# Kernel optimization log

Measured on AMD Instinct MI355X. Metric: run time of the kernel, lower is better.

## Reference

```python
import jax, jax.numpy as jnp
import numpy as np
from jax.ops import segment_sum

EPS = 1e-5
N, E = 100000, 1600000
CIN, H, COUT, ED = 32, 64, 16, 16


def _lin(k, fan_in, fan_out):
    return jax.random.normal(k, (fan_in, fan_out), jnp.float32) / np.sqrt(fan_in)


def setup_inputs() -> dict:
    key = jax.random.key(0)
    ks = jax.random.split(key, 24)
    inp = {
        "x": jax.random.normal(ks[0], (N, CIN), jnp.float32),
        "edge_index": jax.random.randint(ks[1], (2, E), 0, N, jnp.int32),
        "edge_attr": jax.random.normal(ks[2], (E, ED), jnp.float32),
    }
    # layer 1 (SAGEConvWithEdgeAttr: in=CIN -> H)
    inp.update(
        l1_Wl=_lin(ks[3], CIN, H), l1_bl=jnp.zeros((H,), jnp.float32),
        l1_Wr=_lin(ks[4], CIN, H),
        l1_We=_lin(ks[5], ED, H), l1_be=jnp.zeros((H,), jnp.float32),
        l1_Wg=_lin(ks[6], 2 * H, H), l1_bg=jnp.zeros((H,), jnp.float32),
        l1_bng=jnp.ones((H,), jnp.float32), l1_bnb=jnp.zeros((H,), jnp.float32),
    )
    # layer 2 (H -> H)
    inp.update(
        l2_Wl=_lin(ks[7], H, H), l2_bl=jnp.zeros((H,), jnp.float32),
        l2_Wr=_lin(ks[8], H, H),
        l2_We=_lin(ks[9], ED, H), l2_be=jnp.zeros((H,), jnp.float32),
        l2_Wg=_lin(ks[10], 2 * H, H), l2_bg=jnp.zeros((H,), jnp.float32),
        l2_bng=jnp.ones((H,), jnp.float32), l2_bnb=jnp.zeros((H,), jnp.float32),
    )
    # GraphNorms (weight=1, bias=0, mean_scale=1 at init; randomize slightly via ones)
    inp.update(
        gn1_g=jnp.ones((H,), jnp.float32), gn1_b=jnp.zeros((H,), jnp.float32), gn1_a=jnp.ones((H,), jnp.float32),
        gn2_g=jnp.ones((H,), jnp.float32), gn2_b=jnp.zeros((H,), jnp.float32), gn2_a=jnp.ones((H,), jnp.float32),
        lin_W=_lin(ks[11], H, COUT), lin_b=jnp.zeros((COUT,), jnp.float32),
    )
    return inp


def _sage_edge_layer(x, row, col, ea, Wl, bl, Wr, We, be, Wg, bg, bng, bnb):
    n = x.shape[0]
    ea_t = ea @ We + be                                        # [E', H]
    deg = segment_sum(jnp.ones_like(col, dtype=x.dtype), col, num_segments=n)
    agg = segment_sum(x[row], col, num_segments=n) / jnp.maximum(deg, 1.0)[:, None]
    out = agg @ Wl + bl + x @ Wr                               # SAGEConv (mean)
    gate = jax.nn.sigmoid(jnp.concatenate([out[col], ea_t], -1) @ Wg + bg)
    out = out + segment_sum(gate * ea_t, col, num_segments=n)  # edge contributions
    mu = out.mean(0)
    var = ((out - mu) ** 2).mean(0)                            # BatchNorm1d (batch stats)
    out = bng * (out - mu) * jax.lax.rsqrt(var + EPS) + bnb
    return jax.nn.relu(2.0 * out)                              # Identity residual + out, relu


def _graph_norm(x, g, b, a):
    mu = x.mean(0)
    xc = x - a * mu
    var = (xc ** 2).mean(0)
    return g * xc * jax.lax.rsqrt(var + EPS) + b


def reference(x, edge_index, edge_attr,
              l1_Wl, l1_bl, l1_Wr, l1_We, l1_be, l1_Wg, l1_bg, l1_bng, l1_bnb,
              l2_Wl, l2_bl, l2_Wr, l2_We, l2_be, l2_Wg, l2_bg, l2_bng, l2_bnb,
              gn1_g, gn1_b, gn1_a, gn2_g, gn2_b, gn2_a, lin_W, lin_b):
    n = x.shape[0]
    loop = jnp.arange(n, dtype=edge_index.dtype)
    row = jnp.concatenate([edge_index[0], loop])               # add_self_loops
    col = jnp.concatenate([edge_index[1], loop])
    ea = jnp.concatenate([edge_attr, jnp.ones((n, edge_attr.shape[1]), edge_attr.dtype)], 0)
    h = _sage_edge_layer(x, row, col, ea, l1_Wl, l1_bl, l1_Wr, l1_We, l1_be, l1_Wg, l1_bg, l1_bng, l1_bnb)
    h = jax.nn.relu(h)
    h = jax.nn.relu(_graph_norm(h, gn1_g, gn1_b, gn1_a))
    h = _sage_edge_layer(h, row, col, ea, l2_Wl, l2_bl, l2_Wr, l2_We, l2_be, l2_Wg, l2_bg, l2_bng, l2_bnb)
    h = jax.nn.relu(h)
    h = jax.nn.relu(_graph_norm(h, gn2_g, gn2_b, gn2_a))
    return h @ lin_W + lin_b
```

## Files before the change

kernel.cpp:

```cpp
#include <hip/hip_runtime.h>
#include <hip/hip_fp16.h>
#include <math.h>
#include <stdint.h>

#define H 64
#define ED 16
#define CO 16
#define WGRID 2048
#define NWAVES (WGRID * 4)
#define CPART 2048
static constexpr float EPSV = 1e-5f;
static constexpr float LOG2E = 1.44269504f;

typedef _Float16 h2v __attribute__((ext_vector_type(2)));

__device__ __forceinline__ float sigm2(float z) {
    return __builtin_amdgcn_rcpf(1.0f + __builtin_amdgcn_exp2f(-z));
}

__device__ __forceinline__ h2v as_h2(int x) { union { int i; h2v h; } u; u.i = x; return u.h; }

__device__ __forceinline__ int pack2(float a, float b) {
    __half2 h = __floats2half2_rn(a, b);
    return *reinterpret_cast<int*>(&h);
}

__global__ void k_prep(const float* __restrict__ We1, const float* __restrict__ be1, const float* __restrict__ Wg1,
                       const float* __restrict__ We2, const float* __restrict__ be2, const float* __restrict__ Wg2,
                       float* __restrict__ ws) {
    int j = threadIdx.x;
    for (int l = 0; l < 2; ++l) {
        const float* We = l ? We2 : We1;
        const float* be = l ? be2 : be1;
        const float* Wg = l ? Wg2 : Wg1;
        int* wth = (int*)(ws + (l ? 1024 : 0));
        int* wgh = (int*)(ws + (l ? 1536 : 512));
        float* ets = ws + 2048 + l * 192;
        float* vs  = ws + 2112 + l * 192;
        float* dv  = ws + 2176 + l * 192;
        float wt[ED], wg[ED];
        float et = be[j];
        for (int k = 0; k < ED; ++k) { wt[k] = We[k * H + j]; et += wt[k]; }
        ets[j] = et;
        float d = 0.f;
        for (int m = 0; m < H; ++m) d += be[m] * Wg[(H + m) * H + j];
        float vsum = d;
        for (int k = 0; k < ED; ++k) {
            float acc = 0.f;
            for (int m = 0; m < H; ++m) acc += We[k * H + m] * Wg[(H + m) * H + j];
            wg[k] = acc;
            vsum += acc;
        }
        dv[j] = d * LOG2E;
        vs[j] = vsum * LOG2E;
        for (int q = 0; q < 8; ++q) {
            wth[j * 8 + q] = pack2(wt[2 * q], wt[2 * q + 1]);
            wgh[j * 8 + q] = pack2(wg[2 * q] * LOG2E, wg[2 * q + 1] * LOG2E);
        }
    }
    for (int s = 0; s < 8; ++s) ws[2432 + s * 64 + j] = 0.f;
}

__global__ void k_xh(const float* __restrict__ x, __half* __restrict__ xh, int total4) {
    int i = blockIdx.x * blockDim.x + threadIdx.x;
    if (i >= total4) return;
    float4 v = *reinterpret_cast<const float4*>(x + (size_t)i * 4);
    __half2 h0 = __floats2half2_rn(v.x, v.y), h1 = __floats2half2_rn(v.z, v.w);
    uint2 o;
    o.x = *reinterpret_cast<unsigned*>(&h0);
    o.y = *reinterpret_cast<unsigned*>(&h1);
    *reinterpret_cast<uint2*>(xh + (size_t)i * 4) = o;
}

__global__ void k_eah(const float* __restrict__ ea, int4* __restrict__ eah, int E) {
    int e = blockIdx.x * blockDim.x + threadIdx.x;
    if (e >= E) return;
    const float4* src = reinterpret_cast<const float4*>(ea + (size_t)e * ED);
    float4 v0 = src[0], v1 = src[1], v2 = src[2], v3 = src[3];
    int hh[8];
    hh[0] = pack2(v0.x, v0.y); hh[1] = pack2(v0.z, v0.w);
    hh[2] = pack2(v1.x, v1.y); hh[3] = pack2(v1.z, v1.w);
    hh[4] = pack2(v2.x, v2.y); hh[5] = pack2(v2.z, v2.w);
    hh[6] = pack2(v3.x, v3.y); hh[7] = pack2(v3.z, v3.w);
    const int4* o = reinterpret_cast<const int4*>(hh);
    eah[(size_t)e * 2 + 0] = o[0];
    eah[(size_t)e * 2 + 1] = o[1];
}

__global__ void k_count(const int* __restrict__ cols, int* __restrict__ cnt, int E) {
    int e = blockIdx.x * blockDim.x + threadIdx.x;
    if (e < E) atomicAdd(&cnt[cols[e]], 1);
}

__global__ __launch_bounds__(1024) void k_scan1(const int* __restrict__ cnt, int* __restrict__ bs, int N) {
    __shared__ int ls[1024];
    int t = threadIdx.x;
    int i = blockIdx.x * 1024 + t;
    ls[t] = (i < N) ? cnt[i] : 0;
    __syncthreads();
    for (int off = 512; off > 0; off >>= 1) {
        if (t < off) ls[t] += ls[t + off];
        __syncthreads();
    }
    if (t == 0) bs[blockIdx.x] = ls[0];
}

__global__ __launch_bounds__(1024) void k_scan2(int* __restrict__ bs, int SB) {
    __shared__ int ls[1024];
    int t = threadIdx.x;
    int v = (t < SB) ? bs[t] : 0;
    ls[t] = v;
    __syncthreads();
    for (int off = 1; off < 1024; off <<= 1) {
        int x = (t >= off) ? ls[t - off] : 0;
        __syncthreads();
        ls[t] += x;
        __syncthreads();
    }
    if (t < SB) bs[t] = ls[t] - v;
}

__global__ __launch_bounds__(1024) void k_scan3(const int* __restrict__ cnt, const int* __restrict__ bs,
                                                int* __restrict__ rowptr, int N, int E) {
    __shared__ int ls[1024];
    int t = threadIdx.x;
    int i = blockIdx.x * 1024 + t;
    int v = (i < N) ? cnt[i] : 0;
    ls[t] = v;
    __syncthreads();
    for (int off = 1; off < 1024; off <<= 1) {
        int x = (t >= off) ? ls[t - off] : 0;
        __syncthreads();
        ls[t] += x;
        __syncthreads();
    }
    if (i < N) rowptr[i] = bs[blockIdx.x] + ls[t] - v;
    if (i == 0) rowptr[N] = E;
}

__global__ void k_ranges(const int* __restrict__ rowptr, int* __restrict__ ranges, int N, int E, int nw) {
    int w = blockIdx.x * blockDim.x + threadIdx.x;
    if (w > nw) return;
    if (w == nw) { ranges[nw] = N; return; }
    int t0 = (int)((long)E * w / nw);
    int lo = 0, hi = N;
    while (lo < hi) { int mid = (lo + hi) >> 1; if (rowptr[mid] < t0) lo = mid + 1; else hi = mid; }
    ranges[w] = lo;
}

__global__ __launch_bounds__(256) void k_part(const int* __restrict__ rows, const int* __restrict__ cols,
                                              int2* __restrict__ tmp, int* __restrict__ offtab,
                                              int E, int NB, int SH) {
    __shared__ int hist[1025];
    __shared__ int pscan[256];
    __shared__ int2 stage[CPART];
    int tid = threadIdx.x;
    int base = blockIdx.x * CPART;
    int cnt = min(CPART, E - base);
    for (int i = tid; i <= NB; i += 256) hist[i] = 0;
    __syncthreads();
    int myc[8], myr[8];
#pragma unroll
    for (int q = 0; q < 8; ++q) {
        int li = q * 256 + tid;
        if (li < cnt) {
            int e = base + li;
            myc[q] = cols[e];
            myr[q] = rows[e];
            atomicAdd(&hist[myc[q] >> SH], 1);
        } else myc[q] = -1;
    }
    __syncthreads();
    int h[4], s = 0;
    int b0 = tid * 4;
#pragma unroll
    for (int k = 0; k < 4; ++k) { h[k] = (b0 + k < NB) ? hist[b0 + k] : 0; s += h[k]; }
    pscan[tid] = s;
    __syncthreads();
    for (int off = 1; off < 256; off <<= 1) {
        int v = (tid >= off) ? pscan[tid - off] : 0;
        __syncthreads();
        pscan[tid] += v;
        __syncthreads();
    }
    int excl = pscan[tid] - s;
    __syncthreads();
    int run = excl;
#pragma unroll
    for (int k = 0; k < 4; ++k) {
        if (b0 + k < NB) hist[b0 + k] = run;
        run += h[k];
    }
    __syncthreads();
    int* ot = offtab + (size_t)blockIdx.x * (NB + 1);
    for (int i = tid; i < NB; i += 256) ot[i] = hist[i];
    if (tid == 0) ot[NB] = cnt;
    __syncthreads();
    int mask = (1 << SH) - 1;
#pragma unroll
    for (int q = 0; q < 8; ++q) {
        if (myc[q] >= 0) {
            int b = myc[q] >> SH;
            int p = atomicAdd(&hist[b], 1);
            int e = base + q * 256 + tid;
            stage[p] = make_int2(myr[q], (e << SH) | (myc[q] & mask));
        }
    }
    __syncthreads();
    int2* dst = tmp + base;
    for (int i = tid; i < cnt; i += 256) dst[i] = stage[i];
}

__global__ __launch_bounds__(256) void k_build(const int* __restrict__ rowptr, const int2* __restrict__ tmp,
                                               const int* __restrict__ offtab, const int4* __restrict__ eah,
                                               int* __restrict__ erow, __half* __restrict__ eap,
                                               int N, int NB, int SH, int PB) {
    __shared__ int lcur[1024];
    int tid = threadIdx.x;
    int b = blockIdx.x;
    int NPB = 1 << SH;
    int nodelo = b << SH;
    for (int j = tid; j < NPB; j += 256) {
        int n = nodelo + j;
        lcur[j] = (n < N) ? rowptr[n] : 0;
    }
    __syncthreads();
    int mask = NPB - 1;
    for (int i = tid; i < PB; i += 256) {
        const int* ot = offtab + (size_t)i * (NB + 1);
        int j0 = ot[b], j1 = ot[b + 1];
        for (int j = j0; j < j1; ++j) {
            int2 v = tmp[(size_t)i * CPART + j];
            int e = (int)(((unsigned)v.y) >> SH);
            int cl = v.y & mask;
            int p = atomicAdd(&lcur[cl], 1);
            erow[p] = v.x;
            int4 a0 = eah[(size_t)e * 2 + 0];
            int4 a1 = eah[(size_t)e * 2 + 1];
            int4* d = reinterpret_cast<int4*>(eap + (size_t)p * ED);
            d[0] = a0; d[1] = a1;
        }
    }
}

template <int CIN, bool GN>
__global__ __launch_bounds__(256) void k_gather(const __half* __restrict__ x, const int* __restrict__ rowptr,
                         const int* __restrict__ ranges,
                         const int* __restrict__ erow, float* __restrict__ agg,
                         const float* __restrict__ s1, const float* __restrict__ s2,
                         const float* __restrict__ gng, const float* __restrict__ gnb,
                         const float* __restrict__ gna, float Ninv, int N) {
    int lane = threadIdx.x & 63;
    int w = (blockIdx.x * blockDim.x + threadIdx.x) >> 6;
    float A = 1.f, B = 0.f;
    if (GN) {
        float mu = s1[lane] * Ninv, m2 = s2[lane] * Ninv, a = gna[lane];
        float var = m2 - 2.f * a * mu * mu + a * a * mu * mu;
        A = gng[lane] * rsqrtf(var + EPSV);
        B = gnb[lane] - A * a * mu;
    }
    int n0 = ranges[w], n1 = ranges[w + 1];
    for (int n = n0; n < n1; ++n) {
        int s = rowptr[n], te = rowptr[n + 1];
        if (CIN == 64) {
            float raw = __half2float(x[(size_t)n * 64 + lane]);
            float acc = GN ? fmaxf(fmaf(A, raw, B), 0.f) : raw;
            int i = s;
            for (; i + 7 < te; i += 8) {
                int r0 = erow[i],     r1 = erow[i + 1], r2 = erow[i + 2], r3 = erow[i + 3];
                int r4 = erow[i + 4], r5 = erow[i + 5], r6 = erow[i + 6], r7 = erow[i + 7];
                float x0 = __half2float(x[(size_t)r0 * 64 + lane]);
                float x1 = __half2float(x[(size_t)r1 * 64 + lane]);
                float x2 = __half2float(x[(size_t)r2 * 64 + lane]);
                float x3 = __half2float(x[(size_t)r3 * 64 + lane]);
                float x4 = __half2float(x[(size_t)r4 * 64 + lane]);
                float x5 = __half2float(x[(size_t)r5 * 64 + lane]);
                float x6 = __half2float(x[(size_t)r6 * 64 + lane]);
                float x7 = __half2float(x[(size_t)r7 * 64 + lane]);
                if (GN) {
                    x0 = fmaxf(fmaf(A, x0, B), 0.f); x1 = fmaxf(fmaf(A, x1, B), 0.f);
                    x2 = fmaxf(fmaf(A, x2, B), 0.f); x3 = fmaxf(fmaf(A, x3, B), 0.f);
                    x4 = fmaxf(fmaf(A, x4, B), 0.f); x5 = fmaxf(fmaf(A, x5, B), 0.f);
                    x6 = fmaxf(fmaf(A, x6, B), 0.f); x7 = fmaxf(fmaf(A, x7, B), 0.f);
                }
                acc += ((x0 + x1) + (x2 + x3)) + ((x4 + x5) + (x6 + x7));
            }
            for (; i < te; ++i) {
                float xv = __half2float(x[(size_t)erow[i] * 64 + lane]);
                if (GN) xv = fmaxf(fmaf(A, xv, B), 0.f);
                acc += xv;
            }
            agg[(size_t)n * H + lane] = acc;
        } else {
            int c = lane & 31, half = lane >> 5;
            float acc = half ? 0.f : __half2float(x[(size_t)n * 32 + c]);
            int i = s + half;
            for (; i + 6 < te; i += 8) {
                int r0 = erow[i], r1 = erow[i + 2], r2 = erow[i + 4], r3 = erow[i + 6];
                float x0 = __half2float(x[(size_t)r0 * 32 + c]);
                float x1 = __half2float(x[(size_t)r1 * 32 + c]);
                float x2 = __half2float(x[(size_t)r2 * 32 + c]);
                float x3 = __half2float(x[(size_t)r3 * 32 + c]);
                acc += (x0 + x1) + (x2 + x3);
            }
            for (; i < te; i += 2) acc += __half2float(x[(size_t)erow[i] * 32 + c]);
            acc += __shfl_xor(acc, 32);
            if (half == 0) agg[(size_t)n * H + c] = acc;
        }
    }
}

#define MT4A(mq, aval) \
    acc[mq][0] = fmaf(aval, w1.x, acc[mq][0]); acc[mq][1] = fmaf(aval, w1.y, acc[mq][1]); \
    acc[mq][2] = fmaf(aval, w1.z, acc[mq][2]); acc[mq][3] = fmaf(aval, w1.w, acc[mq][3]);
#define MT4X(mq, aval) \
    acc[mq][0] = fmaf(aval, w2.x, acc[mq][0]); acc[mq][1] = fmaf(aval, w2.y, acc[mq][1]); \
    acc[mq][2] = fmaf(aval, w2.z, acc[mq][2]); acc[mq][3] = fmaf(aval, w2.w, acc[mq][3]);

template <int K, bool GN>
__global__ __launch_bounds__(256) void k_gemmfu(
        const float* __restrict__ A,
        const __half* __restrict__ A2, int lda2,
        const float* __restrict__ W1, const float* __restrict__ W2,
        const float* __restrict__ bias,
        const float* __restrict__ Wg, const float* __restrict__ bg,
        const float* __restrict__ s1, const float* __restrict__ s2,
        const float* __restrict__ gng, const float* __restrict__ gnb,
        const float* __restrict__ gna, float Ninv,
        const int* __restrict__ rowptr,
        __half* __restrict__ pre, __half* __restrict__ uout, int N) {
    __shared__ float WA[64 * 64];
    __shared__ float WB[K * 64];
    __shared__ float big[64][68];
    __shared__ float As[64], Bs[64], invd[64];
    int tid = threadIdx.x;
    for (int idx = tid; idx < K * 64; idx += 256) { WA[idx] = W1[idx]; WB[idx] = W2[idx]; }
    int nb = blockIdx.x * 64;
    if (tid < 64) {
        if (GN) {
            float mu = s1[tid] * Ninv, m2 = s2[tid] * Ninv, a = gna[tid];
            float var = m2 - 2.f * a * mu * mu + a * a * mu * mu;
            float Av = gng[tid] * rsqrtf(var + EPSV);
            As[tid] = Av; Bs[tid] = gnb[tid] - Av * a * mu;
        }
        int n = nb + tid;
        invd[tid] = (n < N) ? 1.f / (float)(rowptr[n + 1] - rowptr[n] + 1) : 0.f;
    }
    __syncthreads();
    int tm = tid >> 4, tn = tid & 15;
    int m0 = tm * 4, j0 = tn * 4;
    float acc[4][4];
#pragma unroll
    for (int jq = 0; jq < 4; ++jq) {
        float b = bias[j0 + jq];
#pragma unroll
        for (int mq = 0; mq < 4; ++mq) acc[mq][jq] = b;
    }
    int sn = tid >> 2, kq4 = (tid & 3) * 4;
    int sg = nb + sn;
    for (int k0 = 0; k0 < K; k0 += 16) {
        if (k0) __syncthreads();
        if (sg < N) {
            float4 av = *reinterpret_cast<const float4*>(A + (size_t)sg * 64 + k0 + kq4);
            float sc = invd[sn];
            av.x *= sc; av.y *= sc; av.z *= sc; av.w *= sc;
            big[kq4 + 0][sn] = av.x; big[kq4 + 1][sn] = av.y;
            big[kq4 + 2][sn] = av.z; big[kq4 + 3][sn] = av.w;
            uint2 hv = *reinterpret_cast<const uint2*>(A2 + (size_t)sg * lda2 + k0 + kq4);
            __half2 h01 = *reinterpret_cast<__half2*>(&hv.x);
            __half2 h23 = *reinterpret_cast<__half2*>(&hv.y);
            float2 f01 = __half22float2(h01), f23 = __half22float2(h23);
            float xv0 = f01.x, xv1 = f01.y, xv2 = f23.x, xv3 = f23.y;
            if (GN) {
                xv0 = fmaxf(fmaf(As[k0 + kq4 + 0], xv0, Bs[k0 + kq4 + 0]), 0.f);
                xv1 = fmaxf(fmaf(As[k0 + kq4 + 1], xv1, Bs[k0 + kq4 + 1]), 0.f);
                xv2 = fmaxf(fmaf(As[k0 + kq4 + 2], xv2, Bs[k0 + kq4 + 2]), 0.f);
                xv3 = fmaxf(fmaf(As[k0 + kq4 + 3], xv3, Bs[k0 + kq4 + 3]), 0.f);
            }
            big[16 + kq4 + 0][sn] = xv0; big[16 + kq4 + 1][sn] = xv1;
            big[16 + kq4 + 2][sn] = xv2; big[16 + kq4 + 3][sn] = xv3;
        } else {
#pragma unroll
            for (int q = 0; q < 4; ++q) { big[kq4 + q][sn] = 0.f; big[16 + kq4 + q][sn] = 0.f; }
        }
        __syncthreads();
#pragma unroll
        for (int k = 0; k < 16; ++k) {
            float4 am = *reinterpret_cast<const float4*>(&big[k][m0]);
            float4 w1 = *reinterpret_cast<const float4*>(&WA[(k0 + k) * 64 + j0]);
            MT4A(0, am.x) MT4A(1, am.y) MT4A(2, am.z) MT4A(3, am.w)
            float4 xm = *reinterpret_cast<const float4*>(&big[16 + k][m0]);
            float4 w2 = *reinterpret_cast<const float4*>(&WB[(k0 + k) * 64 + j0]);
            MT4X(0, xm.x) MT4X(1, xm.y) MT4X(2, xm.z) MT4X(3, xm.w)
        }
    }
    __syncthreads();
#pragma unroll
    for (int mq = 0; mq < 4; ++mq) {
        int n = nb + m0 + mq;
        if (n < N) {
            uint2 o;
            o.x = pack2(acc[mq][0], acc[mq][1]);
            o.y = pack2(acc[mq][2], acc[mq][3]);
            *reinterpret_cast<uint2*>(pre + (size_t)n * 64 + j0) = o;
        }
#pragma unroll
        for (int jq = 0; jq < 4; ++jq) big[j0 + jq][m0 + mq] = acc[mq][jq];
    }
    for (int idx = tid; idx < 4096; idx += 256) WA[idx] = Wg[idx] * LOG2E;
    __syncthreads();
    float acc2[4][4];
#pragma unroll
    for (int jq = 0; jq < 4; ++jq) {
        float b = bg[j0 + jq] * LOG2E;
#pragma unroll
        for (int mq = 0; mq < 4; ++mq) acc2[mq][jq] = b;
    }
#pragma unroll 8
    for (int k = 0; k < 64; ++k) {
        float4 pm = *reinterpret_cast<const float4*>(&big[k][m0]);
        float4 w1 = *reinterpret_cast<const float4*>(&WA[k * 64 + j0]);
        acc2[0][0] = fmaf(pm.x, w1.x, acc2[0][0]); acc2[0][1] = fmaf(pm.x, w1.y, acc2[0][1]);
        acc2[0][2] = fmaf(pm.x, w1.z, acc2[0][2]); acc2[0][3] = fmaf(pm.x, w1.w, acc2[0][3]);
        acc2[1][0] = fmaf(pm.y, w1.x, acc2[1][0]); acc2[1][1] = fmaf(pm.y, w1.y, acc2[1][1]);
        acc2[1][2] = fmaf(pm.y, w1.z, acc2[1][2]); acc2[1][3] = fmaf(pm.y, w1.w, acc2[1][3]);
        acc2[2][0] = fmaf(pm.z, w1.x, acc2[2][0]); acc2[2][1] = fmaf(pm.z, w1.y, acc2[2][1]);
        acc2[2][2] = fmaf(pm.z, w1.z, acc2[2][2]); acc2[2][3] = fmaf(pm.z, w1.w, acc2[2][3]);
        acc2[3][0] = fmaf(pm.w, w1.x, acc2[3][0]); acc2[3][1] = fmaf(pm.w, w1.y, acc2[3][1]);
        acc2[3][2] = fmaf(pm.w, w1.z, acc2[3][2]); acc2[3][3] = fmaf(pm.w, w1.w, acc2[3][3]);
    }
#pragma unroll
    for (int mq = 0; mq < 4; ++mq) {
        int n = nb + m0 + mq;
        if (n < N) {
            uint2 o;
            o.x = pack2(acc2[mq][0], acc2[mq][1]);
            o.y = pack2(acc2[mq][2], acc2[mq][3]);
            *reinterpret_cast<uint2*>(uout + (size_t)n * 64 + j0) = o;
        }
    }
}

__device__ __forceinline__ float edge_term(const int4& a, const int4& b,
                                           const h2v* wt, const h2v* wg,
                                           float be_l, float dv_l, float u_l) {
    float et = be_l, v = dv_l;
    et = __builtin_amdgcn_fdot2(as_h2(a.x), wt[0], et, false);
    v  = __builtin_amdgcn_fdot2(as_h2(a.x), wg[0], v,  false);
    et = __builtin_amdgcn_fdot2(as_h2(a.y), wt[1], et, false);
    v  = __builtin_amdgcn_fdot2(as_h2(a.y), wg[1], v,  false);
    et = __builtin_amdgcn_fdot2(as_h2(a.z), wt[2], et, false);
    v  = __builtin_amdgcn_fdot2(as_h2(a.z), wg[2], v,  false);
    et = __builtin_amdgcn_fdot2(as_h2(a.w), wt[3], et, false);
    v  = __builtin_amdgcn_fdot2(as_h2(a.w), wg[3], v,  false);
    et = __builtin_amdgcn_fdot2(as_h2(b.x), wt[4], et, false);
    v  = __builtin_amdgcn_fdot2(as_h2(b.x), wg[4], v,  false);
    et = __builtin_amdgcn_fdot2(as_h2(b.y), wt[5], et, false);
    v  = __builtin_amdgcn_fdot2(as_h2(b.y), wg[5], v,  false);
    et = __builtin_amdgcn_fdot2(as_h2(b.z), wt[6], et, false);
    v  = __builtin_amdgcn_fdot2(as_h2(b.z), wg[6], v,  false);
    et = __builtin_amdgcn_fdot2(as_h2(b.w), wt[7], et, false);
    v  = __builtin_amdgcn_fdot2(as_h2(b.w), wg[7], v,  false);
    return sigm2(u_l + v) * et;
}

__global__ __launch_bounds__(256) void k_gate(
        const int* __restrict__ rowptr, const int* __restrict__ ranges,
        const __half* __restrict__ eap,
        const int* __restrict__ wth, const int* __restrict__ wgh,
        const float* __restrict__ be, const float* __restrict__ dv,
        const float* __restrict__ ets, const float* __restrict__ vs,
        const __half* __restrict__ u, __half* __restrict__ pre,
        float* __restrict__ s1, float* __restrict__ s2, int N) {
    __shared__ __align__(16) int4 estage[4][128];
    __shared__ float ls[2][4][H];
    int lane = threadIdx.x & 63;
    int wv = threadIdx.x >> 6;
    int w = (blockIdx.x << 2) | wv;
    h2v wt[8], wg[8];
#pragma unroll
    for (int q = 0; q < 8; ++q) { wt[q] = as_h2(wth[lane * 8 + q]); wg[q] = as_h2(wgh[lane * 8 + q]); }
    float be_l = be[lane], dv_l = dv[lane], ets_l = ets[lane], vs_l = vs[lane];
    int n0 = ranges[w], n1 = ranges[w + 1];
    float s = 0.f, ss = 0.f;
    if (n0 < n1) {
        int4* dst = &estage[wv][0];
        const int4* gsrc = reinterpret_cast<const int4*>(eap);
        int e0 = rowptr[n0], e1 = rowptr[n1];
        int n = n0;
        int nend = rowptr[n0 + 1];
        size_t idx = (size_t)n * H + lane;
        float u_l = __half2float(u[idx]);
        float pv = __half2float(pre[idx]);
        int np = min(n + 1, n1 - 1);
        size_t idxn = (size_t)np * H + lane;
        float u_n = __half2float(u[idxn]);
        float pv_n = __half2float(pre[idxn]);
        float acc = sigm2(u_l + vs_l) * ets_l;
        {
            int bytes = min(64, e1 - e0) * 32;
            int4 p0, p1;
            if (lane * 16 < bytes) p0 = gsrc[(size_t)e0 * 2 + lane];
            if (1024 + lane * 16 < bytes) p1 = gsrc[(size_t)e0 * 2 + 64 + lane];
            if (lane * 16 < bytes) dst[lane] = p0;
            if (1024 + lane * 16 < bytes) dst[64 + lane] = p1;
        }
        for (int c = e0; c < e1; c += 64) {
            int cnt = min(64, e1 - c);
            int nbytes = (c + 64 < e1) ? min(64, e1 - c - 64) * 32 : 0;
            int4 p0, p1;
            if (lane * 16 < nbytes) p0 = gsrc[(size_t)(c + 64) * 2 + lane];
            if (1024 + lane * 16 < nbytes) p1 = gsrc[(size_t)(c + 64) * 2 + 64 + lane];
            int k = 0;
            while (k < cnt) {
                while (c + k == nend) {
                    float tval = pv + acc;
                    pre[idx] = __float2half(tval);
                    s += tval; ss += tval * tval;
                    ++n;
                    idx = idxn; u_l = u_n; pv = pv_n;
                    np = min(n + 1, n1 - 1);
                    idxn = (size_t)np * H + lane;
                    u_n = __half2float(u[idxn]);
                    pv_n = __half2float(pre[idxn]);
                    acc = sigm2(u_l + vs_l) * ets_l;
                    nend = rowptr[n + 1];
                }
                int safe = min(cnt, nend - c);
                for (; k + 1 < safe; k += 2) {
                    int4 d0 = dst[k * 2], d1 = dst[k * 2 + 1];
                    int4 d2 = dst[k * 2 + 2], d3 = dst[k * 2 + 3];
                    acc += edge_term(d0, d1, wt, wg, be_l, dv_l, u_l);
                    acc += edge_term(d2, d3, wt, wg, be_l, dv_l, u_l);
                }
                if (k < safe) {
                    int4 d0 = dst[k * 2], d1 = dst[k * 2 + 1];
                    acc += edge_term(d0, d1, wt, wg, be_l, dv_l, u_l);
                    ++k;
                }
            }
            if (lane * 16 < nbytes) dst[lane] = p0;
            if (1024 + lane * 16 < nbytes) dst[64 + lane] = p1;
        }
        for (;;) {
            float tval = pv + acc;
            pre[idx] = __float2half(tval);
            s += tval; ss += tval * tval;
            ++n;
            if (n >= n1) break;
            idx = idxn; u_l = u_n; pv = pv_n;
            np = min(n + 1, n1 - 1);
            idxn = (size_t)np * H + lane;
            u_n = __half2float(u[idxn]);
            pv_n = __half2float(pre[idxn]);
            acc = sigm2(u_l + vs_l) * ets_l;
        }
    }
    ls[0][wv][lane] = s; ls[1][wv][lane] = ss;
    __syncthreads();
    if (threadIdx.x < H) {
        float a = ls[0][0][lane] + ls[0][1][lane] + ls[0][2][lane] + ls[0][3][lane];
        float b = ls[1][0][lane] + ls[1][1][lane] + ls[1][2][lane] + ls[1][3][lane];
        atomicAdd(&s1[lane], a);
        atomicAdd(&s2[lane], b);
    }
}

__global__ void k_apply(const __half* __restrict__ in, __half* __restrict__ outb,
                        const float* __restrict__ bng, const float* __restrict__ bnb,
                        const float* __restrict__ s1b, const float* __restrict__ s2b,
                        float* __restrict__ s1g, float* __restrict__ s2g, float Ninv, int N) {
    int j = threadIdx.x, ty = threadIdx.y;
    __shared__ float As[H], Bs[H];
    if (ty == 0) {
        float mu = s1b[j] * Ninv, var = s2b[j] * Ninv - mu * mu;
        float r = rsqrtf(var + EPSV);
        float A = 2.f * bng[j] * r;
        As[j] = A; Bs[j] = 2.f * (bnb[j] - bng[j] * r * mu);
    }
    __syncthreads();
    float A = As[j], B = Bs[j];
    float s = 0.f, ss = 0.f;
    for (int n = blockIdx.x * 4 + ty; n < N; n += gridDim.x * 4) {
        size_t idx = (size_t)n * H + j;
        float v = fmaxf(fmaf(A, __half2float(in[idx]), B), 0.f);
        outb[idx] = __float2half(v);
        s += v; ss += v * v;
    }
    __shared__ float ls[2][4][H];
    ls[0][ty][j] = s; ls[1][ty][j] = ss;
    __syncthreads();
    if (ty == 0) {
        float a = ls[0][0][j] + ls[0][1][j] + ls[0][2][j] + ls[0][3][j];
        float b = ls[1][0][j] + ls[1][1][j] + ls[1][2][j] + ls[1][3][j];
        atomicAdd(&s1g[j], a);
        atomicAdd(&s2g[j], b);
    }
}

__global__ __launch_bounds__(256) void k_final(const __half* __restrict__ hraw, const float* __restrict__ W,
                        const float* __restrict__ bias,
                        const float* __restrict__ s1, const float* __restrict__ s2,
                        const float* __restrict__ gng, const float* __restrict__ gnb,
                        const float* __restrict__ gna, float Ninv,
                        float* __restrict__ outp, int N) {
    __shared__ float As[H], Bs[H];
    if (threadIdx.x < H) {
        int j = threadIdx.x;
        float mu = s1[j] * Ninv, m2 = s2[j] * Ninv, a = gna[j];
        float var = m2 - 2.f * a * mu * mu + a * a * mu * mu;
        float A = gng[j] * rsqrtf(var + EPSV);
        As[j] = A; Bs[j] = gnb[j] - A * a * mu;
    }
    __syncthreads();
    int n = blockIdx.x * blockDim.x + threadIdx.x;
    if (n >= N) return;
    float o[CO];
#pragma unroll
    for (int t = 0; t < CO; ++t) o[t] = bias[t];
    const __half* hr = hraw + (size_t)n * H;
    for (int m4 = 0; m4 < H / 4; ++m4) {
        uint2 hv = *reinterpret_cast<const uint2*>(hr + m4 * 4);
        __half2 h01 = *reinterpret_cast<__half2*>(&hv.x);
        __half2 h23 = *reinterpret_cast<__half2*>(&hv.y);
        float2 f01 = __half22float2(h01), f23 = __half22float2(h23);
        float hx = fmaxf(fmaf(As[m4*4+0], f01.x, Bs[m4*4+0]), 0.f);
        float hy = fmaxf(fmaf(As[m4*4+1], f01.y, Bs[m4*4+1]), 0.f);
        float hz = fmaxf(fmaf(As[m4*4+2], f23.x, Bs[m4*4+2]), 0.f);
        float hw = fmaxf(fmaf(As[m4*4+3], f23.y, Bs[m4*4+3]), 0.f);
#pragma unroll
        for (int t = 0; t < CO; ++t) {
            o[t] += hx * W[(m4*4+0) * CO + t];
            o[t] += hy * W[(m4*4+1) * CO + t];
            o[t] += hz * W[(m4*4+2) * CO + t];
            o[t] += hw * W[(m4*4+3) * CO + t];
        }
    }
    float* orow = outp + (size_t)n * CO;
#pragma unroll
    for (int t4 = 0; t4 < CO / 4; ++t4)
        reinterpret_cast<float4*>(orow)[t4] = make_float4(o[t4*4+0], o[t4*4+1], o[t4*4+2], o[t4*4+3]);
}

extern "C" void kernel_launch(void* const* d_in, const int* in_sizes, int n_in,
                              void* d_out, int out_size, void* d_ws, size_t ws_size,
                              hipStream_t stream) {
    const float* x     = (const float*)d_in[0];
    const int*   ei    = (const int*)d_in[1];
    const float* ea    = (const float*)d_in[2];
    const float* l1_Wl = (const float*)d_in[3];  const float* l1_bl = (const float*)d_in[4];
    const float* l1_Wr = (const float*)d_in[5];  const float* l1_We = (const float*)d_in[6];
    const float* l1_be = (const float*)d_in[7];  const float* l1_Wg = (const float*)d_in[8];
    const float* l1_bg = (const float*)d_in[9];  const float* l1_bng= (const float*)d_in[10];
    const float* l1_bnb= (const float*)d_in[11];
    const float* l2_Wl = (const float*)d_in[12]; const float* l2_bl = (const float*)d_in[13];
    const float* l2_Wr = (const float*)d_in[14]; const float* l2_We = (const float*)d_in[15];
    const float* l2_be = (const float*)d_in[16]; const float* l2_Wg = (const float*)d_in[17];
    const float* l2_bg = (const float*)d_in[18]; const float* l2_bng= (const float*)d_in[19];
    const float* l2_bnb= (const float*)d_in[20];
    const float* gn1_g = (const float*)d_in[21]; const float* gn1_b = (const float*)d_in[22];
    const float* gn1_a = (const float*)d_in[23];
    const float* gn2_g = (const float*)d_in[24]; const float* gn2_b = (const float*)d_in[25];
    const float* gn2_a = (const float*)d_in[26];
    const float* lin_W = (const float*)d_in[27]; const float* lin_b = (const float*)d_in[28];

    const int N = in_sizes[0] / 32;
    const int E = in_sizes[1] / 2;
    const int* rows = ei;
    const int* cols = ei + E;

    int SH = 7, NPB = 128;
    while (((N + NPB - 1) >> SH) > 1024) { SH++; NPB <<= 1; }
    const int NB = (N + NPB - 1) >> SH;
    const int PB = (E + CPART - 1) / CPART;

    float* w    = (float*)d_ws;
    int* wth1   = (int*)w;
    int* wgh1   = (int*)(w + 512);
    int* wth2   = (int*)(w + 1024);
    int* wgh2   = (int*)(w + 1536);
    float* ets1 = w + 2048; float* vs1 = w + 2112; float* dv1 = w + 2176;
    float* ets2 = w + 2240; float* vs2 = w + 2304; float* dv2 = w + 2368;
    float* stats= w + 2432;

    int* ip     = (int*)(w + 8192);
    int* rowptr = ip;
    int* cnt    = ip + (N + 1);
    int* bs     = cnt + N;
    int* ranges = bs + 1024;
    int* erow   = ranges + (NWAVES + 2);

    uintptr_t pa = (uintptr_t)(erow + E);
    pa = (pa + 255) & ~(uintptr_t)255;
    __half* eap = (__half*)pa;
    uintptr_t px = (uintptr_t)(eap + (size_t)E * ED);
    px = (px + 255) & ~(uintptr_t)255;
    __half* xh = (__half*)px;
    uintptr_t pz = (uintptr_t)(xh + (size_t)N * 32);
    pz = (pz + 255) & ~(uintptr_t)255;

    int2* tmp   = (int2*)pz;
    int* offtab = (int*)(tmp + E);
    uintptr_t pe = (uintptr_t)(offtab + (size_t)PB * (NB + 1));
    pe = (pe + 255) & ~(uintptr_t)255;
    int4* eah = (int4*)pe;

    size_t NB64 = (size_t)N * H;
    float* B0 = (float*)pz;
    __half* Bpre = (__half*)(B0 + NB64);
    __half* Bu   = Bpre + NB64;
    __half* B3h  = Bu + NB64;
    __half* B0h  = (__half*)B0;

    const float Ninv = 1.0f / (float)N;
    dim3 rb(64, 4);
    int egrid = (E + 255) / 256;
    int ngrid = (N + 255) / 256;
    int g64 = (N + 63) / 64;
    const int SB = (N + 1023) >> 10;

    k_prep<<<1, 64, 0, stream>>>(l1_We, l1_be, l1_Wg, l2_We, l2_be, l2_Wg, w);
    k_xh<<<(N * 8 + 255) / 256, 256, 0, stream>>>(x, xh, N * 8);
    k_eah<<<egrid, 256, 0, stream>>>(ea, eah, E);

    hipMemsetAsync(cnt, 0, sizeof(int) * (size_t)N, stream);
    k_count<<<egrid, 256, 0, stream>>>(cols, cnt, E);
    k_scan1<<<SB, 1024, 0, stream>>>(cnt, bs, N);
    k_scan2<<<1, 1024, 0, stream>>>(bs, SB);
    k_scan3<<<SB, 1024, 0, stream>>>(cnt, bs, rowptr, N, E);
    k_ranges<<<(NWAVES + 256) / 256, 256, 0, stream>>>(rowptr, ranges, N, E, NWAVES);
    k_part<<<PB, 256, 0, stream>>>(rows, cols, tmp, offtab, E, NB, SH);
    k_build<<<NB, 256, 0, stream>>>(rowptr, tmp, offtab, eah, erow, eap, N, NB, SH, PB);

    k_gather<32, false><<<WGRID, 256, 0, stream>>>(xh, rowptr, ranges, erow, B0,
                                                   nullptr, nullptr, nullptr, nullptr, nullptr, 0.f, N);
    k_gemmfu<32, false><<<g64, 256, 0, stream>>>(B0, xh, 32, l1_Wl, l1_Wr, l1_bl, l1_Wg, l1_bg,
                                                 nullptr, nullptr, nullptr, nullptr, nullptr, 0.f,
                                                 rowptr, Bpre, Bu, N);
    k_gate<<<WGRID, 256, 0, stream>>>(rowptr, ranges, eap, wth1, wgh1, l1_be, dv1, ets1, vs1,
                                      Bu, Bpre, stats + 0, stats + 64, N);
    k_apply<<<256, rb, 0, stream>>>(Bpre, B3h, l1_bng, l1_bnb, stats + 0, stats + 64,
                                    stats + 128, stats + 192, Ninv, N);

    k_gather<64, true><<<WGRID, 256, 0, stream>>>(B3h, rowptr, ranges, erow, B0,
                                                  stats + 128, stats + 192, gn1_g, gn1_b, gn1_a, Ninv, N);
    k_gemmfu<64, true><<<g64, 256, 0, stream>>>(B0, B3h, 64, l2_Wl, l2_Wr, l2_bl, l2_Wg, l2_bg,
                                                stats + 128, stats + 192, gn1_g, gn1_b, gn1_a, Ninv,
                                                rowptr, Bpre, Bu, N);
    k_gate<<<WGRID, 256, 0, stream>>>(rowptr, ranges, eap, wth2, wgh2, l2_be, dv2, ets2, vs2,
                                      Bu, Bpre, stats + 256, stats + 320, N);
    k_apply<<<256, rb, 0, stream>>>(Bpre, B0h, l2_bng, l2_bnb, stats + 256, stats + 320,
                                    stats + 384, stats + 448, Ninv, N);

    k_final<<<ngrid, 256, 0, stream>>>(B0h, lin_W, lin_b, stats + 384, stats + 448,
                                       gn2_g, gn2_b, gn2_a, Ninv, (float*)d_out, N);
}
```

Before: 713.0 us.

## Compute per-edge attr projections in k_gate with MFMA tiles via LDS

Replaces the per-lane fdot2 chains for the edge-attribute projections (et and gate v) with 16x16x32 f16 MFMA over 16-edge tiles. The results are staged through per-wave LDS buffers and then consumed by the existing segment-walking accumulation loop. The aim is to cut VALU dot-product work on the hot edge loop. In exchange it adds LDS round-trips, half the lanes feed zeros into the MFMA K dimension, and it uses more shared memory, which may reduce occupancy.

```diff
diff --git a/kernel.cpp b/kernel.cpp
--- a/kernel.cpp
+++ b/kernel.cpp
@@ -13,12 +13,16 @@
 static constexpr float LOG2E = 1.44269504f;
 
 typedef _Float16 h2v __attribute__((ext_vector_type(2)));
+typedef _Float16 f16x8 __attribute__((ext_vector_type(8)));
+typedef float f32x4 __attribute__((ext_vector_type(4)));
 
 __device__ __forceinline__ float sigm2(float z) {
     return __builtin_amdgcn_rcpf(1.0f + __builtin_amdgcn_exp2f(-z));
 }
 
 __device__ __forceinline__ h2v as_h2(int x) { union { int i; h2v h; } u; u.i = x; return u.h; }
+
+__device__ __forceinline__ f16x8 as_f16x8(int4 v) { union { int4 i; f16x8 h; } u; u.i = v; return u.h; }
 
 __device__ __forceinline__ int pack2(float a, float b) {
     __half2 h = __floats2half2_rn(a, b);
@@ -441,29 +445,6 @@
     }
 }
 
-__device__ __forceinline__ float edge_term(const int4& a, const int4& b,
-                                           const h2v* wt, const h2v* wg,
-                                           float be_l, float dv_l, float u_l) {
-    float et = be_l, v = dv_l;
-    et = __builtin_amdgcn_fdot2(as_h2(a.x), wt[0], et, false);
-    v  = __builtin_amdgcn_fdot2(as_h2(a.x), wg[0], v,  false);
-    et = __builtin_amdgcn_fdot2(as_h2(a.y), wt[1], et, false);
-    v  = __builtin_amdgcn_fdot2(as_h2(a.y), wg[1], v,  false);
-    et = __builtin_amdgcn_fdot2(as_h2(a.z), wt[2], et, false);
-    v  = __builtin_amdgcn_fdot2(as_h2(a.z), wg[2], v,  false);
-    et = __builtin_amdgcn_fdot2(as_h2(a.w), wt[3], et, false);
-    v  = __builtin_amdgcn_fdot2(as_h2(a.w), wg[3], v,  false);
-    et = __builtin_amdgcn_fdot2(as_h2(b.x), wt[4], et, false);
-    v  = __builtin_amdgcn_fdot2(as_h2(b.x), wg[4], v,  false);
-    et = __builtin_amdgcn_fdot2(as_h2(b.y), wt[5], et, false);
-    v  = __builtin_amdgcn_fdot2(as_h2(b.y), wg[5], v,  false);
-    et = __builtin_amdgcn_fdot2(as_h2(b.z), wt[6], et, false);
-    v  = __builtin_amdgcn_fdot2(as_h2(b.z), wg[6], v,  false);
-    et = __builtin_amdgcn_fdot2(as_h2(b.w), wt[7], et, false);
-    v  = __builtin_amdgcn_fdot2(as_h2(b.w), wg[7], v,  false);
-    return sigm2(u_l + v) * et;
-}
-
 __global__ __launch_bounds__(256) void k_gate(
         const int* __restrict__ rowptr, const int* __restrict__ ranges,
         const __half* __restrict__ eap,
@@ -473,13 +454,25 @@
         const __half* __restrict__ u, __half* __restrict__ pre,
         float* __restrict__ s1, float* __restrict__ s2, int N) {
     __shared__ __align__(16) int4 estage[4][128];
+    __shared__ float vbuf[4][16][68];
+    __shared__ float ebuf[4][16][68];
     __shared__ float ls[2][4][H];
     int lane = threadIdx.x & 63;
     int wv = threadIdx.x >> 6;
     int w = (blockIdx.x << 2) | wv;
-    h2v wt[8], wg[8];
-#pragma unroll
-    for (int q = 0; q < 8; ++q) { wt[q] = as_h2(wth[lane * 8 + q]); wg[q] = as_h2(wgh[lane * 8 + q]); }
+    int g = lane >> 4, li = lane & 15;
+    f16x8 Bet[4], Bv[4];
+#pragma unroll
+    for (int c = 0; c < 4; ++c) {
+        int j = c * 16 + li;
+        int4 bt = make_int4(0, 0, 0, 0), bv = make_int4(0, 0, 0, 0);
+        if (g < 2) {
+            bt = *reinterpret_cast<const int4*>(&wth[j * 8 + g * 4]);
+            bv = *reinterpret_cast<const int4*>(&wgh[j * 8 + g * 4]);
+        }
+        Bet[c] = as_f16x8(bt);
+        Bv[c] = as_f16x8(bv);
+    }
     float be_l = be[lane], dv_l = dv[lane], ets_l = ets[lane], vs_l = vs[lane];
     int n0 = ranges[w], n1 = ranges[w + 1];
     float s = 0.f, ss = 0.f;
@@ -497,6 +490,7 @@
         float u_n = __half2float(u[idxn]);
         float pv_n = __half2float(pre[idxn]);
         float acc = sigm2(u_l + vs_l) * ets_l;
+        float u2 = u_l + dv_l;
         {
             int bytes = min(64, e1 - e0) * 32;
             int4 p0, p1;
@@ -511,32 +505,61 @@
             int4 p0, p1;
             if (lane * 16 < nbytes) p0 = gsrc[(size_t)(c + 64) * 2 + lane];
             if (1024 + lane * 16 < nbytes) p1 = gsrc[(size_t)(c + 64) * 2 + 64 + lane];
-            int k = 0;
-            while (k < cnt) {
-                while (c + k == nend) {
-                    float tval = pv + acc;
-                    pre[idx] = __float2half(tval);
-                    s += tval; ss += tval * tval;
-                    ++n;
-                    idx = idxn; u_l = u_n; pv = pv_n;
-                    np = min(n + 1, n1 - 1);
-                    idxn = (size_t)np * H + lane;
-                    u_n = __half2float(u[idxn]);
-                    pv_n = __half2float(pre[idxn]);
-                    acc = sigm2(u_l + vs_l) * ets_l;
-                    nend = rowptr[n + 1];
+            for (int tb = 0; tb < cnt; tb += 16) {
+                int4 af = make_int4(0, 0, 0, 0);
+                if (g < 2) af = dst[(tb + li) * 2 + g];
+                f16x8 Af = as_f16x8(af);
+                f32x4 z = {0.f, 0.f, 0.f, 0.f};
+                f32x4 et0 = __builtin_amdgcn_mfma_f32_16x16x32_f16(Af, Bet[0], z, 0, 0, 0);
+                f32x4 et1 = __builtin_amdgcn_mfma_f32_16x16x32_f16(Af, Bet[1], z, 0, 0, 0);
+                f32x4 et2 = __builtin_amdgcn_mfma_f32_16x16x32_f16(Af, Bet[2], z, 0, 0, 0);
+                f32x4 et3 = __builtin_amdgcn_mfma_f32_16x16x32_f16(Af, Bet[3], z, 0, 0, 0);
+                f32x4 vv0 = __builtin_amdgcn_mfma_f32_16x16x32_f16(Af, Bv[0], z, 0, 0, 0);
+                f32x4 vv1 = __builtin_amdgcn_mfma_f32_16x16x32_f16(Af, Bv[1], z, 0, 0, 0);
+                f32x4 vv2 = __builtin_amdgcn_mfma_f32_16x16x32_f16(Af, Bv[2], z, 0, 0, 0);
+                f32x4 vv3 = __builtin_amdgcn_mfma_f32_16x16x32_f16(Af, Bv[3], z, 0, 0, 0);
+                int r0 = g * 4;
+#pragma unroll
+                for (int r = 0; r < 4; ++r) {
+                    ebuf[wv][r0 + r][li]      = et0[r];
+                    ebuf[wv][r0 + r][16 + li] = et1[r];
+                    ebuf[wv][r0 + r][32 + li] = et2[r];
+                    ebuf[wv][r0 + r][48 + li] = et3[r];
+                    vbuf[wv][r0 + r][li]      = vv0[r];
+                    vbuf[wv][r0 + r][16 + li] = vv1[r];
+                    vbuf[wv][r0 + r][32 + li] = vv2[r];
+                    vbuf[wv][r0 + r][48 + li] = vv3[r];
                 }
-                int safe = min(cnt, nend - c);
-                for (; k + 1 < safe; k += 2) {
-                    int4 d0 = dst[k * 2], d1 = dst[k * 2 + 1];
-                    int4 d2 = dst[k * 2 + 2], d3 = dst[k * 2 + 3];
-                    acc += edge_term(d0, d1, wt, wg, be_l, dv_l, u_l);
-                    acc += edge_term(d2, d3, wt, wg, be_l, dv_l, u_l);
-                }
-                if (k < safe) {
-                    int4 d0 = dst[k * 2], d1 = dst[k * 2 + 1];
-                    acc += edge_term(d0, d1, wt, wg, be_l, dv_l, u_l);
-                    ++k;
+                int p = tb, pend = min(cnt, tb + 16);
+                while (p < pend) {
+                    while (c + p == nend) {
+                        float tval = pv + acc;
+                        pre[idx] = __float2half(tval);
+                        s += tval; ss += tval * tval;
+                        ++n;
+                        idx = idxn; u_l = u_n; pv = pv_n;
+                        np = min(n + 1, n1 - 1);
+                        idxn = (size_t)np * H + lane;
+                        u_n = __half2float(u[idxn]);
+                        pv_n = __half2float(pre[idxn]);
+                        acc = sigm2(u_l + vs_l) * ets_l;
+                        u2 = u_l + dv_l;
+                        nend = rowptr[n + 1];
+                    }
+                    int lim = min(pend, nend - c);
+                    for (; p + 1 < lim; p += 2) {
+                        float V0 = vbuf[wv][p - tb][lane];
+                        float E0 = ebuf[wv][p - tb][lane];
+                        float V1 = vbuf[wv][p + 1 - tb][lane];
+                        float E1 = ebuf[wv][p + 1 - tb][lane];
+                        acc += sigm2(u2 + V0) * (be_l + E0) + sigm2(u2 + V1) * (be_l + E1);
+                    }
+                    if (p < lim) {
+                        float V0 = vbuf[wv][p - tb][lane];
+                        float E0 = ebuf[wv][p - tb][lane];
+                        acc += sigm2(u2 + V0) * (be_l + E0);
+                        ++p;
+                    }
                 }
             }
             if (lane * 16 < nbytes) dst[lane] = p0;
@@ -554,6 +577,7 @@
             u_n = __half2float(u[idxn]);
             pv_n = __half2float(pre[idxn]);
             acc = sigm2(u_l + vs_l) * ets_l;
+            u2 = u_l + dv_l;
         }
     }
     ls[0][wv][lane] = s; ls[1][wv][lane] = ss;
```

After: 695.4 us. 1.03x faster.
